# Optimization experiments

Hardware: AMD Instinct MI355X
Metric: run time of the kernel (lower is better)

The kernel has to match this reference:

```python
import jax, jax.numpy as jnp
import numpy as np

D_IN = 1024
D_OUT = 1024


def setup_inputs() -> dict:
    key = jax.random.key(0)
    k_x, k_q, k_k, k_v = jax.random.split(key, 4)
    x = jax.random.normal(k_x, (8, 2048, D_IN), dtype=jnp.float32)
    s = 1.0 / np.sqrt(D_IN)
    W_query = jax.random.uniform(k_q, (D_IN, D_OUT), jnp.float32, -s, s)
    W_key = jax.random.uniform(k_k, (D_IN, D_OUT), jnp.float32, -s, s)
    W_value = jax.random.uniform(k_v, (D_IN, D_OUT), jnp.float32, -s, s)
    return {"x": x, "W_query": W_query, "W_key": W_key, "W_value": W_value}


def reference(x, W_query, W_key, W_value):
    # x: [B, N, d_in]; weights stored as [d_in, d_out] (already transposed vs torch Linear)
    B, N, _ = x.shape
    q = x @ W_query          # [B, N, d_out]
    k = x @ W_key
    v = x @ W_value
    scores = jnp.einsum('bnd,bmd->bnm', q, k)  # [B, N, N]
    causal = jnp.tril(jnp.ones((N, N), dtype=bool))
    scores = jnp.where(causal, scores, -jnp.inf)
    weights = jax.nn.softmax(scores / np.sqrt(D_OUT), axis=-1)
    # dropout p=0.0 -> identity
    return jnp.einsum('bnm,bmd->bnd', weights, v)
```

## Files before the change

### kernel.cpp

```cpp
#include <hip/hip_runtime.h>
#include <hip/hip_bf16.h>

typedef unsigned short u16;
typedef unsigned int u32;
typedef __bf16 bf16x8 __attribute__((ext_vector_type(8)));
typedef float f32x4 __attribute__((ext_vector_type(4)));
typedef unsigned int u32x4 __attribute__((ext_vector_type(4)));

#define BATCH 8
#define SEQ   2048
#define DIM   1024
#define M_TOT (BATCH * SEQ)
#define N_QKV (3 * DIM)

#define OFF_QKV  ((size_t)0)
#define OFF_VT   ((size_t)100663296)
#define OFF_C    ((size_t)134217728)
#define OFF_XB   OFF_C
#define OFF_WT   (OFF_C + (size_t)33554432)
#define OFF_S    OFF_C

__device__ __forceinline__ u16 f32_to_bf16(float f) {
    u32 u = __builtin_bit_cast(u32, f);
    u = (u + 0x7fffu + ((u >> 16) & 1u)) >> 16;
    return (u16)u;
}

__device__ __forceinline__ float bf16_to_f32(u16 h) {
    u32 u = ((u32)h) << 16;
    return __builtin_bit_cast(float, u);
}

__device__ __forceinline__ bf16x8 lds_load8(const u16* p) {
    return __builtin_bit_cast(bf16x8, *(const u32x4*)p);
}

__device__ __forceinline__ void stage_tile64(const u16* gA, size_t lda, u16* ldsA, int tid) {
    int wv = tid >> 6;
#pragma unroll
    for (int iss = 0; iss < 4; ++iss) {
        int s = iss * 256 + tid;
        int row = s >> 3;
        int kg = (s & 7) ^ (row & 7);
        const u16* gp = gA + (size_t)row * lda + (kg << 3);
        u16* lp = ldsA + (size_t)(iss * 256 + wv * 64) * 8;
        __builtin_amdgcn_global_load_lds((const __attribute__((address_space(1))) void*)gp,
                                         (__attribute__((address_space(3))) void*)lp,
                                         16, 0, 0);
    }
}

__device__ __forceinline__ void mfma_step64(const u16* ldsA, const u16* ldsB, int tid,
                                            f32x4 acc[4][4]) {
    int lane = tid & 63;
    int wv = tid >> 6;
    int wr = (wv >> 1) * 64, wc = (wv & 1) * 64;
    int lrow = lane & 15, kgl = lane >> 4;
    int xr = lrow & 7;
#pragma unroll
    for (int ks = 0; ks < 2; ++ks) {
        int off = ((ks * 4 + kgl) ^ xr) << 3;
        bf16x8 a[4], b[4];
#pragma unroll
        for (int i = 0; i < 4; ++i) {
            a[i] = lds_load8(&ldsA[(wr + i * 16 + lrow) * 64 + off]);
            b[i] = lds_load8(&ldsB[(wc + i * 16 + lrow) * 64 + off]);
        }
#pragma unroll
        for (int i = 0; i < 4; ++i)
#pragma unroll
            for (int j = 0; j < 4; ++j)
                acc[i][j] = __builtin_amdgcn_mfma_f32_16x16x32_bf16(a[i], b[j], acc[i][j], 0, 0, 0);
    }
}

__global__ __launch_bounds__(256) void cast_x_kernel(const float* __restrict__ x,
                                                     u16* __restrict__ xb) {
    size_t g = (size_t)blockIdx.x * 256 + threadIdx.x;
    f32x4 v = ((const f32x4*)x)[g];
    u16 o[4] = {f32_to_bf16(v.x), f32_to_bf16(v.y), f32_to_bf16(v.z), f32_to_bf16(v.w)};
    *(unsigned long long*)(xb + g * 4) = *(const unsigned long long*)o;
}

__global__ __launch_bounds__(256) void transpose_w_kernel(const float* __restrict__ wq,
                                                          const float* __restrict__ wk,
                                                          const float* __restrict__ wv,
                                                          u16* __restrict__ wt) {
    __shared__ __align__(16) u16 tile[64][80];
    const float* w = blockIdx.z == 0 ? wq : (blockIdx.z == 1 ? wk : wv);
    int k0 = blockIdx.x * 64, n0 = blockIdx.y * 64;
    for (int g = threadIdx.x; g < 1024; g += 256) {
        int r = g >> 4, c = (g & 15) << 2;
        f32x4 v = *(const f32x4*)(w + (size_t)(k0 + r) * 1024 + n0 + c);
        tile[r][c + 0] = f32_to_bf16(v.x);
        tile[r][c + 1] = f32_to_bf16(v.y);
        tile[r][c + 2] = f32_to_bf16(v.z);
        tile[r][c + 3] = f32_to_bf16(v.w);
    }
    __syncthreads();
    u16* out = wt + (size_t)blockIdx.z * 1024 * 1024;
    for (int g = threadIdx.x; g < 512; g += 256) {
        int nr = g >> 3, kc = (g & 7) << 3;
        __align__(16) u16 tmp[8];
#pragma unroll
        for (int i = 0; i < 8; ++i) tmp[i] = tile[kc + i][nr];
        *(u32x4*)(out + (size_t)(n0 + nr) * 1024 + k0 + kc) = *(const u32x4*)tmp;
    }
}

__global__ __launch_bounds__(256, 2) void gemm_qkv_kernel(const u16* __restrict__ xb,
                                                          const u16* __restrict__ wt,
                                                          u16* __restrict__ qkv) {
    __shared__ __align__(16) u16 ldsA[128 * 64];
    __shared__ __align__(16) u16 ldsB[128 * 64];
    int nt = blockIdx.x, mt = blockIdx.y;
    const u16* A = xb + (size_t)mt * 128 * 1024;
    const u16* B = wt + (size_t)nt * 128 * 1024;
    int tid = threadIdx.x;
    f32x4 acc[4][4] = {};
    for (int kt = 0; kt < 16; ++kt) {
        __syncthreads();
        stage_tile64(A + kt * 64, 1024, ldsA, tid);
        stage_tile64(B + kt * 64, 1024, ldsB, tid);
        __syncthreads();
        mfma_step64(ldsA, ldsB, tid, acc);
    }
    int lane = tid & 63, wv = tid >> 6;
    int wr = (wv >> 1) * 64, wc = (wv & 1) * 64;
    int r0 = (lane >> 4) * 4, c0 = lane & 15;
    size_t mbase = (size_t)mt * 128;
    int nbase = nt * 128;
#pragma unroll
    for (int i = 0; i < 4; ++i)
#pragma unroll
        for (int j = 0; j < 4; ++j) {
            int col = nbase + wc + j * 16 + c0;
            float scale = (col < 1024) ? 0.03125f : 1.0f;
#pragma unroll
            for (int r = 0; r < 4; ++r) {
                int row = wr + i * 16 + r0 + r;
                qkv[(mbase + row) * (size_t)N_QKV + col] = f32_to_bf16(acc[i][j][r] * scale);
            }
        }
}

__global__ __launch_bounds__(256) void transpose_v_kernel(const u16* __restrict__ qkv,
                                                          u16* __restrict__ vt) {
    __shared__ __align__(16) u16 tile[64][80];
    int m0 = blockIdx.x * 64, d0 = blockIdx.y * 64, b = blockIdx.z;
    const u16* src = qkv + (size_t)b * SEQ * N_QKV + 2048;
    for (int g = threadIdx.x; g < 512; g += 256) {
        int r = g >> 3, c = (g & 7) << 3;
        *(u32x4*)&tile[r][c] = *(const u32x4*)(src + (size_t)(m0 + r) * N_QKV + d0 + c);
    }
    __syncthreads();
    u16* dst = vt + (size_t)b * DIM * SEQ;
    for (int g = threadIdx.x; g < 512; g += 256) {
        int dr = g >> 3, mc = (g & 7) << 3;
        __align__(16) u16 tmp[8];
#pragma unroll
        for (int i = 0; i < 8; ++i) tmp[i] = tile[mc + i][dr];
        *(u32x4*)(dst + (size_t)(d0 + dr) * SEQ + m0 + mc) = *(const u32x4*)tmp;
    }
}

__global__ __launch_bounds__(256, 2) void gemm_scores_kernel(const u16* __restrict__ qkv,
                                                             u16* __restrict__ S) {
    int t = blockIdx.x;
    int b = blockIdx.y;
    int ntile = (int)((sqrtf(8.0f * (float)t + 1.0f) - 1.0f) * 0.5f);
    while ((ntile + 1) * (ntile + 2) / 2 <= t) ++ntile;
    while (ntile * (ntile + 1) / 2 > t) --ntile;
    int mtile = t - ntile * (ntile + 1) / 2;
    __shared__ __align__(16) u16 ldsA[128 * 64];
    __shared__ __align__(16) u16 ldsB[128 * 64];
    const u16* A = qkv + (size_t)b * SEQ * N_QKV + (size_t)ntile * 128 * N_QKV;
    const u16* B = qkv + (size_t)b * SEQ * N_QKV + (size_t)mtile * 128 * N_QKV + 1024;
    int tid = threadIdx.x;
    f32x4 acc[4][4] = {};
    for (int kt = 0; kt < 16; ++kt) {
        __syncthreads();
        stage_tile64(A + kt * 64, N_QKV, ldsA, tid);
        stage_tile64(B + kt * 64, N_QKV, ldsB, tid);
        __syncthreads();
        mfma_step64(ldsA, ldsB, tid, acc);
    }
    u16* out = S + (size_t)b * SEQ * SEQ + (size_t)ntile * 128 * SEQ + (size_t)mtile * 128;
    int lane = tid & 63, wv = tid >> 6;
    int wr = (wv >> 1) * 64, wc = (wv & 1) * 64;
    int r0 = (lane >> 4) * 4, c0 = lane & 15;
#pragma unroll
    for (int i = 0; i < 4; ++i)
#pragma unroll
        for (int j = 0; j < 4; ++j) {
            int col = wc + j * 16 + c0;
#pragma unroll
            for (int r = 0; r < 4; ++r) {
                int row = wr + i * 16 + r0 + r;
                out[(size_t)row * SEQ + col] = f32_to_bf16(acc[i][j][r]);
            }
        }
}

__global__ __launch_bounds__(256) void softmax_kernel(u16* __restrict__ SP) {
    int gr = blockIdx.x;
    int n = gr & 2047;
    u16* s = SP + (size_t)gr * SEQ;
    __shared__ float red[4];
    int t = threadIdx.x;
    int base = t << 3;
    int len = n + 1;
    float v[8];
    float lmax = -3.0e38f;
    if (base < len) {
        u32x4 raw = *(const u32x4*)(s + base);
        const u16* h = (const u16*)&raw;
#pragma unroll
        for (int i = 0; i < 8; ++i) {
            v[i] = (base + i < len) ? bf16_to_f32(h[i]) : -3.0e38f;
            lmax = fmaxf(lmax, v[i]);
        }
    } else {
#pragma unroll
        for (int i = 0; i < 8; ++i) v[i] = -3.0e38f;
    }
#pragma unroll
    for (int off = 32; off; off >>= 1) lmax = fmaxf(lmax, __shfl_xor(lmax, off, 64));
    if ((t & 63) == 0) red[t >> 6] = lmax;
    __syncthreads();
    float gmax = fmaxf(fmaxf(red[0], red[1]), fmaxf(red[2], red[3]));
    __syncthreads();
    float lsum = 0.f;
#pragma unroll
    for (int i = 0; i < 8; ++i) {
        float e = __expf(v[i] - gmax);
        v[i] = e;
        lsum += e;
    }
#pragma unroll
    for (int off = 32; off; off >>= 1) lsum += __shfl_xor(lsum, off, 64);
    if ((t & 63) == 0) red[t >> 6] = lsum;
    __syncthreads();
    float inv = 1.0f / (red[0] + red[1] + red[2] + red[3]);
    __align__(16) u16 o[8];
#pragma unroll
    for (int i = 0; i < 8; ++i) o[i] = f32_to_bf16(v[i] * inv);
    *(u32x4*)(s + base) = *(const u32x4*)o;
}

__global__ __launch_bounds__(256, 2) void gemm_out_kernel(const u16* __restrict__ P,
                                                          const u16* __restrict__ vt,
                                                          float* __restrict__ O) {
    __shared__ __align__(16) u16 ldsA[128 * 64];
    __shared__ __align__(16) u16 ldsB[128 * 64];
    int dt = blockIdx.x, b = blockIdx.z;
    int ntile = (SEQ / 128 - 1) - blockIdx.y;
    const u16* A = P + (size_t)b * SEQ * SEQ + (size_t)ntile * 128 * SEQ;
    const u16* B = vt + (size_t)b * DIM * SEQ + (size_t)dt * 128 * SEQ;
    int tid = threadIdx.x;
    f32x4 acc[4][4] = {};
    int kTiles = ntile * 2 + 2;
    for (int kt = 0; kt < kTiles; ++kt) {
        __syncthreads();
        stage_tile64(A + kt * 64, SEQ, ldsA, tid);
        stage_tile64(B + kt * 64, SEQ, ldsB, tid);
        __syncthreads();
        mfma_step64(ldsA, ldsB, tid, acc);
    }
    float* out = O + (size_t)b * SEQ * DIM + (size_t)ntile * 128 * DIM + (size_t)dt * 128;
    int lane = tid & 63, wv = tid >> 6;
    int wr = (wv >> 1) * 64, wc = (wv & 1) * 64;
    int r0 = (lane >> 4) * 4, c0 = lane & 15;
#pragma unroll
    for (int i = 0; i < 4; ++i)
#pragma unroll
        for (int j = 0; j < 4; ++j) {
            int col = wc + j * 16 + c0;
#pragma unroll
            for (int r = 0; r < 4; ++r) {
                int row = wr + i * 16 + r0 + r;
                out[(size_t)row * DIM + col] = acc[i][j][r];
            }
        }
}

extern "C" void kernel_launch(void* const* d_in, const int* in_sizes, int n_in,
                              void* d_out, int out_size, void* d_ws, size_t ws_size,
                              hipStream_t stream) {
    const float* x = (const float*)d_in[0];
    const float* wq = (const float*)d_in[1];
    const float* wk = (const float*)d_in[2];
    const float* wv = (const float*)d_in[3];
    char* ws = (char*)d_ws;
    u16* qkv = (u16*)(ws + OFF_QKV);
    u16* vt = (u16*)(ws + OFF_VT);
    u16* xb = (u16*)(ws + OFF_XB);
    u16* wt = (u16*)(ws + OFF_WT);
    u16* S = (u16*)(ws + OFF_S);
    float* O = (float*)d_out;

    cast_x_kernel<<<M_TOT * DIM / 4 / 256, 256, 0, stream>>>(x, xb);
    transpose_w_kernel<<<dim3(16, 16, 3), 256, 0, stream>>>(wq, wk, wv, wt);
    gemm_qkv_kernel<<<dim3(N_QKV / 128, M_TOT / 128), 256, 0, stream>>>(xb, wt, qkv);
    transpose_v_kernel<<<dim3(SEQ / 64, DIM / 64, BATCH), 256, 0, stream>>>(qkv, vt);
    gemm_scores_kernel<<<dim3(136, BATCH), 256, 0, stream>>>(qkv, S);
    softmax_kernel<<<BATCH * SEQ, 256, 0, stream>>>(S);
    gemm_out_kernel<<<dim3(DIM / 128, SEQ / 128, BATCH), 256, 0, stream>>>(S, vt, O);
}
```

Measured before the change: 394.8 us.

## Use 256x256 tiles with double-buffered async LDS pipeline in all GEMMs

Replaces the 128x128 single-buffered GEMM mainloop with a 256x256, 512-thread tile and a double-buffered global_load_lds prefetch pipeline that interleaves staging with MFMA phases, using s_setprio around MFMA bursts. The QKV GEMM also gets an XCD-aware block swizzle. This aims to hide global load latency and raise arithmetic intensity per LDS byte. It uses 128KB LDS per block, which limits occupancy, and the coarser tiles mean fewer blocks (the scores GEMM drops to 36 blocks per batch), risking tail imbalance.

```diff
diff --git a/kernel.cpp b/kernel.cpp
--- a/kernel.cpp
+++ b/kernel.cpp
@@ -35,42 +35,80 @@
     return __builtin_bit_cast(bf16x8, *(const u32x4*)p);
 }
 
-__device__ __forceinline__ void stage_tile64(const u16* gA, size_t lda, u16* ldsA, int tid) {
+#define UNIT 8192
+
+__device__ __forceinline__ void stage_unit(const u16* g, size_t lda, int k0,
+                                           u16* lds, int tid) {
     int wv = tid >> 6;
 #pragma unroll
-    for (int iss = 0; iss < 4; ++iss) {
-        int s = iss * 256 + tid;
-        int row = s >> 3;
-        int kg = (s & 7) ^ (row & 7);
-        const u16* gp = gA + (size_t)row * lda + (kg << 3);
-        u16* lp = ldsA + (size_t)(iss * 256 + wv * 64) * 8;
+    for (int iss = 0; iss < 2; ++iss) {
+        int s = iss * 512 + tid;
+        int row = s >> 2;
+        int kg = (s & 3) ^ (row & 3);
+        const u16* gp = g + (size_t)row * lda + (k0 + (kg << 3));
+        u16* lp = lds + (size_t)(iss * 512 + wv * 64) * 8;
         __builtin_amdgcn_global_load_lds((const __attribute__((address_space(1))) void*)gp,
                                          (__attribute__((address_space(3))) void*)lp,
                                          16, 0, 0);
     }
 }
 
-__device__ __forceinline__ void mfma_step64(const u16* ldsA, const u16* ldsB, int tid,
-                                            f32x4 acc[4][4]) {
+template <int MH>
+__device__ __forceinline__ void mfma_phase(const u16* uA, const u16* uB, int lane,
+                                           int wm, int wn, f32x4 acc[8][4]) {
+    int lrow = lane & 15;
+    int off = (((lane >> 4) ^ (lane & 3)) << 3);
+    bf16x8 a[4], b[4];
+#pragma unroll
+    for (int i = 0; i < 4; ++i) {
+        a[i] = lds_load8(&uA[(wm * 128 + (MH * 4 + i) * 16 + lrow) * 32 + off]);
+        b[i] = lds_load8(&uB[(wn * 64 + i * 16 + lrow) * 32 + off]);
+    }
+    __builtin_amdgcn_s_setprio(1);
+#pragma unroll
+    for (int i = 0; i < 4; ++i)
+#pragma unroll
+        for (int j = 0; j < 4; ++j)
+            acc[MH * 4 + i][j] =
+                __builtin_amdgcn_mfma_f32_16x16x32_bf16(a[i], b[j], acc[MH * 4 + i][j], 0, 0, 0);
+    __builtin_amdgcn_s_setprio(0);
+}
+
+__device__ __forceinline__ void gemm_block_256(const u16* __restrict__ A, size_t lda,
+                                               const u16* __restrict__ B, size_t ldb,
+                                               int KT, u16* lds, int tid,
+                                               f32x4 acc[8][4]) {
     int lane = tid & 63;
     int wv = tid >> 6;
-    int wr = (wv >> 1) * 64, wc = (wv & 1) * 64;
-    int lrow = lane & 15, kgl = lane >> 4;
-    int xr = lrow & 7;
-#pragma unroll
-    for (int ks = 0; ks < 2; ++ks) {
-        int off = ((ks * 4 + kgl) ^ xr) << 3;
-        bf16x8 a[4], b[4];
-#pragma unroll
-        for (int i = 0; i < 4; ++i) {
-            a[i] = lds_load8(&ldsA[(wr + i * 16 + lrow) * 64 + off]);
-            b[i] = lds_load8(&ldsB[(wc + i * 16 + lrow) * 64 + off]);
-        }
-#pragma unroll
-        for (int i = 0; i < 4; ++i)
-#pragma unroll
-            for (int j = 0; j < 4; ++j)
-                acc[i][j] = __builtin_amdgcn_mfma_f32_16x16x32_bf16(a[i], b[j], acc[i][j], 0, 0, 0);
+    int wm = wv >> 2, wn = wv & 3;
+    stage_unit(A, lda, 0,  lds + 0 * UNIT, tid);
+    stage_unit(B, ldb, 0,  lds + 4 * UNIT, tid);
+    stage_unit(A, lda, 32, lds + 1 * UNIT, tid);
+    stage_unit(B, ldb, 32, lds + 5 * UNIT, tid);
+    for (int t = 0; t < KT; ++t) {
+        int p = t & 1, pn = p ^ 1;
+        int kb = (t + 1) << 6;
+        bool pf = (t + 1 < KT);
+        asm volatile("s_waitcnt vmcnt(4)" ::: "memory");
+        __builtin_amdgcn_s_barrier();
+        if (pf) stage_unit(A, lda, kb, lds + (size_t)(pn * 2) * UNIT, tid);
+        mfma_phase<0>(lds + (size_t)(p * 2) * UNIT, lds + (size_t)(4 + p * 2) * UNIT,
+                      lane, wm, wn, acc);
+        __builtin_amdgcn_s_barrier();
+        if (pf) stage_unit(B, ldb, kb, lds + (size_t)(4 + pn * 2) * UNIT, tid);
+        mfma_phase<1>(lds + (size_t)(p * 2) * UNIT, lds + (size_t)(4 + p * 2) * UNIT,
+                      lane, wm, wn, acc);
+        __builtin_amdgcn_s_barrier();
+        if (pf) { asm volatile("s_waitcnt vmcnt(4)" ::: "memory"); }
+        else    { asm volatile("s_waitcnt vmcnt(0)" ::: "memory"); }
+        __builtin_amdgcn_s_barrier();
+        if (pf) stage_unit(A, lda, kb + 32, lds + (size_t)(pn * 2 + 1) * UNIT, tid);
+        mfma_phase<0>(lds + (size_t)(p * 2 + 1) * UNIT, lds + (size_t)(4 + p * 2 + 1) * UNIT,
+                      lane, wm, wn, acc);
+        __builtin_amdgcn_s_barrier();
+        if (pf) stage_unit(B, ldb, kb + 32, lds + (size_t)(4 + pn * 2 + 1) * UNIT, tid);
+        mfma_phase<1>(lds + (size_t)(p * 2 + 1) * UNIT, lds + (size_t)(4 + p * 2 + 1) * UNIT,
+                      lane, wm, wn, acc);
     }
 }
 
@@ -108,38 +146,34 @@
     }
 }
 
-__global__ __launch_bounds__(256, 2) void gemm_qkv_kernel(const u16* __restrict__ xb,
+__global__ __launch_bounds__(512, 2) void gemm_qkv_kernel(const u16* __restrict__ xb,
                                                           const u16* __restrict__ wt,
                                                           u16* __restrict__ qkv) {
-    __shared__ __align__(16) u16 ldsA[128 * 64];
-    __shared__ __align__(16) u16 ldsB[128 * 64];
-    int nt = blockIdx.x, mt = blockIdx.y;
-    const u16* A = xb + (size_t)mt * 128 * 1024;
-    const u16* B = wt + (size_t)nt * 128 * 1024;
+    __shared__ __align__(16) u16 lds[8 * UNIT];
+    int wg = blockIdx.x;
+    int qx = gridDim.x >> 3;
+    int swz = (wg & 7) * qx + (wg >> 3);
+    int mt = swz / 12, nt = swz - mt * 12;
+    const u16* A = xb + (size_t)mt * 256 * 1024;
+    const u16* B = wt + (size_t)nt * 256 * 1024;
     int tid = threadIdx.x;
-    f32x4 acc[4][4] = {};
-    for (int kt = 0; kt < 16; ++kt) {
-        __syncthreads();
-        stage_tile64(A + kt * 64, 1024, ldsA, tid);
-        stage_tile64(B + kt * 64, 1024, ldsB, tid);
-        __syncthreads();
-        mfma_step64(ldsA, ldsB, tid, acc);
-    }
+    f32x4 acc[8][4] = {};
+    gemm_block_256(A, 1024, B, 1024, 16, lds, tid, acc);
     int lane = tid & 63, wv = tid >> 6;
-    int wr = (wv >> 1) * 64, wc = (wv & 1) * 64;
-    int r0 = (lane >> 4) * 4, c0 = lane & 15;
-    size_t mbase = (size_t)mt * 128;
-    int nbase = nt * 128;
-#pragma unroll
-    for (int i = 0; i < 4; ++i)
+    int wm = wv >> 2, wn = wv & 3;
+    int r0 = (lane >> 4) << 2, c0 = lane & 15;
+    size_t mbase = (size_t)mt * 256 + wm * 128;
+    int nbase = nt * 256 + wn * 64;
+#pragma unroll
+    for (int i = 0; i < 8; ++i)
 #pragma unroll
         for (int j = 0; j < 4; ++j) {
-            int col = nbase + wc + j * 16 + c0;
+            int col = nbase + j * 16 + c0;
             float scale = (col < 1024) ? 0.03125f : 1.0f;
 #pragma unroll
             for (int r = 0; r < 4; ++r) {
-                int row = wr + i * 16 + r0 + r;
-                qkv[(mbase + row) * (size_t)N_QKV + col] = f32_to_bf16(acc[i][j][r] * scale);
+                size_t row = mbase + i * 16 + r0 + r;
+                qkv[row * (size_t)N_QKV + col] = f32_to_bf16(acc[i][j][r] * scale);
             }
         }
 }
@@ -164,39 +198,33 @@
     }
 }
 
-__global__ __launch_bounds__(256, 2) void gemm_scores_kernel(const u16* __restrict__ qkv,
+__global__ __launch_bounds__(512, 2) void gemm_scores_kernel(const u16* __restrict__ qkv,
                                                              u16* __restrict__ S) {
+    __shared__ __align__(16) u16 lds[8 * UNIT];
     int t = blockIdx.x;
     int b = blockIdx.y;
-    int ntile = (int)((sqrtf(8.0f * (float)t + 1.0f) - 1.0f) * 0.5f);
-    while ((ntile + 1) * (ntile + 2) / 2 <= t) ++ntile;
-    while (ntile * (ntile + 1) / 2 > t) --ntile;
-    int mtile = t - ntile * (ntile + 1) / 2;
-    __shared__ __align__(16) u16 ldsA[128 * 64];
-    __shared__ __align__(16) u16 ldsB[128 * 64];
-    const u16* A = qkv + (size_t)b * SEQ * N_QKV + (size_t)ntile * 128 * N_QKV;
-    const u16* B = qkv + (size_t)b * SEQ * N_QKV + (size_t)mtile * 128 * N_QKV + 1024;
+    int ntile = 0;
+#pragma unroll
+    for (int it = 1; it < 8; ++it)
+        if ((it * (it + 1)) / 2 <= t) ntile = it;
+    int mtile = t - (ntile * (ntile + 1)) / 2;
+    const u16* A = qkv + (size_t)b * SEQ * N_QKV + (size_t)ntile * 256 * N_QKV;
+    const u16* B = qkv + (size_t)b * SEQ * N_QKV + (size_t)mtile * 256 * N_QKV + 1024;
     int tid = threadIdx.x;
-    f32x4 acc[4][4] = {};
-    for (int kt = 0; kt < 16; ++kt) {
-        __syncthreads();
-        stage_tile64(A + kt * 64, N_QKV, ldsA, tid);
-        stage_tile64(B + kt * 64, N_QKV, ldsB, tid);
-        __syncthreads();
-        mfma_step64(ldsA, ldsB, tid, acc);
-    }
-    u16* out = S + (size_t)b * SEQ * SEQ + (size_t)ntile * 128 * SEQ + (size_t)mtile * 128;
+    f32x4 acc[8][4] = {};
+    gemm_block_256(A, N_QKV, B, N_QKV, 16, lds, tid, acc);
+    u16* out = S + (size_t)b * SEQ * SEQ + (size_t)ntile * 256 * SEQ + (size_t)mtile * 256;
     int lane = tid & 63, wv = tid >> 6;
-    int wr = (wv >> 1) * 64, wc = (wv & 1) * 64;
-    int r0 = (lane >> 4) * 4, c0 = lane & 15;
-#pragma unroll
-    for (int i = 0; i < 4; ++i)
+    int wm = wv >> 2, wn = wv & 3;
+    int r0 = (lane >> 4) << 2, c0 = lane & 15;
+#pragma unroll
+    for (int i = 0; i < 8; ++i)
 #pragma unroll
         for (int j = 0; j < 4; ++j) {
-            int col = wc + j * 16 + c0;
+            int col = wn * 64 + j * 16 + c0;
 #pragma unroll
             for (int r = 0; r < 4; ++r) {
-                int row = wr + i * 16 + r0 + r;
+                int row = wm * 128 + i * 16 + r0 + r;
                 out[(size_t)row * SEQ + col] = f32_to_bf16(acc[i][j][r]);
             }
         }
@@ -248,37 +276,30 @@
     *(u32x4*)(s + base) = *(const u32x4*)o;
 }
 
-__global__ __launch_bounds__(256, 2) void gemm_out_kernel(const u16* __restrict__ P,
+__global__ __launch_bounds__(512, 2) void gemm_out_kernel(const u16* __restrict__ P,
                                                           const u16* __restrict__ vt,
                                                           float* __restrict__ O) {
-    __shared__ __align__(16) u16 ldsA[128 * 64];
-    __shared__ __align__(16) u16 ldsB[128 * 64];
+    __shared__ __align__(16) u16 lds[8 * UNIT];
     int dt = blockIdx.x, b = blockIdx.z;
-    int ntile = (SEQ / 128 - 1) - blockIdx.y;
-    const u16* A = P + (size_t)b * SEQ * SEQ + (size_t)ntile * 128 * SEQ;
-    const u16* B = vt + (size_t)b * DIM * SEQ + (size_t)dt * 128 * SEQ;
+    int ntile = (SEQ / 256 - 1) - blockIdx.y;
+    const u16* A = P + (size_t)b * SEQ * SEQ + (size_t)ntile * 256 * SEQ;
+    const u16* B = vt + (size_t)b * DIM * SEQ + (size_t)dt * 256 * SEQ;
     int tid = threadIdx.x;
-    f32x4 acc[4][4] = {};
-    int kTiles = ntile * 2 + 2;
-    for (int kt = 0; kt < kTiles; ++kt) {
-        __syncthreads();
-        stage_tile64(A + kt * 64, SEQ, ldsA, tid);
-        stage_tile64(B + kt * 64, SEQ, ldsB, tid);
-        __syncthreads();
-        mfma_step64(ldsA, ldsB, tid, acc);
-    }
-    float* out = O + (size_t)b * SEQ * DIM + (size_t)ntile * 128 * DIM + (size_t)dt * 128;
+    f32x4 acc[8][4] = {};
+    int KT = (ntile + 1) * 4;
+    gemm_block_256(A, SEQ, B, SEQ, KT, lds, tid, acc);
+    float* out = O + (size_t)b * SEQ * DIM + (size_t)ntile * 256 * DIM + (size_t)dt * 256;
     int lane = tid & 63, wv = tid >> 6;
-    int wr = (wv >> 1) * 64, wc = (wv & 1) * 64;
-    int r0 = (lane >> 4) * 4, c0 = lane & 15;
-#pragma unroll
-    for (int i = 0; i < 4; ++i)
+    int wm = wv >> 2, wn = wv & 3;
+    int r0 = (lane >> 4) << 2, c0 = lane & 15;
+#pragma unroll
+    for (int i = 0; i < 8; ++i)
 #pragma unroll
         for (int j = 0; j < 4; ++j) {
-            int col = wc + j * 16 + c0;
+            int col = wn * 64 + j * 16 + c0;
 #pragma unroll
             for (int r = 0; r < 4; ++r) {
-                int row = wr + i * 16 + r0 + r;
+                int row = wm * 128 + i * 16 + r0 + r;
                 out[(size_t)row * DIM + col] = acc[i][j][r];
             }
         }
@@ -301,9 +322,9 @@
 
     cast_x_kernel<<<M_TOT * DIM / 4 / 256, 256, 0, stream>>>(x, xb);
     transpose_w_kernel<<<dim3(16, 16, 3), 256, 0, stream>>>(wq, wk, wv, wt);
-    gemm_qkv_kernel<<<dim3(N_QKV / 128, M_TOT / 128), 256, 0, stream>>>(xb, wt, qkv);
+    gemm_qkv_kernel<<<(M_TOT / 256) * (N_QKV / 256), 512, 0, stream>>>(xb, wt, qkv);
     transpose_v_kernel<<<dim3(SEQ / 64, DIM / 64, BATCH), 256, 0, stream>>>(qkv, vt);
-    gemm_scores_kernel<<<dim3(136, BATCH), 256, 0, stream>>>(qkv, S);
+    gemm_scores_kernel<<<dim3(36, BATCH), 512, 0, stream>>>(qkv, S);
     softmax_kernel<<<BATCH * SEQ, 256, 0, stream>>>(S);
-    gemm_out_kernel<<<dim3(DIM / 128, SEQ / 128, BATCH), 256, 0, stream>>>(S, vt, O);
-}
+    gemm_out_kernel<<<dim3(DIM / 256, SEQ / 256, BATCH), 512, 0, stream>>>(S, vt, O);
+}
```

New measurement: 401.9 us. No clear change (+1.8%).

## Double-buffer LDS tiles in all GEMM kernels to overlap loads with MFMA

Applied to the files above, without the earlier changes.

Adds a shared gemm_loop_db helper that prefetches the next K-tile into a second LDS buffer while MFMAs run on the current one. Partial vmcnt waits and raw s_barrier calls replace the two __syncthreads per step in the QKV, scores and output GEMMs. The goal is to hide global-load latency behind matrix math. This doubles LDS per block to 64 KB, which can limit occupancy, and it relies on stage_tile64 issuing a fixed count of vector-memory ops. The triangular tile index in the scores kernel is also recomputed with an unrolled loop instead of sqrtf.

```diff
diff --git a/kernel.cpp b/kernel.cpp
--- a/kernel.cpp
+++ b/kernel.cpp
@@ -19,6 +19,8 @@
 #define OFF_XB   OFF_C
 #define OFF_WT   (OFF_C + (size_t)33554432)
 #define OFF_S    OFF_C
+
+#define TILE_ELEMS (128 * 64)
 
 __device__ __forceinline__ u16 f32_to_bf16(float f) {
     u32 u = __builtin_bit_cast(u32, f);
@@ -71,6 +73,31 @@
 #pragma unroll
             for (int j = 0; j < 4; ++j)
                 acc[i][j] = __builtin_amdgcn_mfma_f32_16x16x32_bf16(a[i], b[j], acc[i][j], 0, 0, 0);
+    }
+}
+
+__device__ __forceinline__ void gemm_loop_db(const u16* __restrict__ A, size_t lda,
+                                             const u16* __restrict__ B, size_t ldb,
+                                             int KT, u16* ldsA, u16* ldsB, int tid,
+                                             f32x4 acc[4][4]) {
+    stage_tile64(A, lda, ldsA, tid);
+    stage_tile64(B, ldb, ldsB, tid);
+    int cur = 0;
+    for (int t = 0; t < KT; ++t) {
+        int nxt = cur ^ 1;
+        if (t + 1 < KT) {
+            stage_tile64(A + (size_t)(t + 1) * 64, lda, ldsA + nxt * TILE_ELEMS, tid);
+            stage_tile64(B + (size_t)(t + 1) * 64, ldb, ldsB + nxt * TILE_ELEMS, tid);
+            asm volatile("s_waitcnt vmcnt(8)" ::: "memory");
+        } else {
+            asm volatile("s_waitcnt vmcnt(0)" ::: "memory");
+        }
+        __builtin_amdgcn_s_barrier();
+        __builtin_amdgcn_sched_barrier(0);
+        mfma_step64(ldsA + cur * TILE_ELEMS, ldsB + cur * TILE_ELEMS, tid, acc);
+        __builtin_amdgcn_s_barrier();
+        __builtin_amdgcn_sched_barrier(0);
+        cur = nxt;
     }
 }
 
@@ -111,20 +138,14 @@
 __global__ __launch_bounds__(256, 2) void gemm_qkv_kernel(const u16* __restrict__ xb,
                                                           const u16* __restrict__ wt,
                                                           u16* __restrict__ qkv) {
-    __shared__ __align__(16) u16 ldsA[128 * 64];
-    __shared__ __align__(16) u16 ldsB[128 * 64];
+    __shared__ __align__(16) u16 ldsA[2 * TILE_ELEMS];
+    __shared__ __align__(16) u16 ldsB[2 * TILE_ELEMS];
     int nt = blockIdx.x, mt = blockIdx.y;
     const u16* A = xb + (size_t)mt * 128 * 1024;
     const u16* B = wt + (size_t)nt * 128 * 1024;
     int tid = threadIdx.x;
     f32x4 acc[4][4] = {};
-    for (int kt = 0; kt < 16; ++kt) {
-        __syncthreads();
-        stage_tile64(A + kt * 64, 1024, ldsA, tid);
-        stage_tile64(B + kt * 64, 1024, ldsB, tid);
-        __syncthreads();
-        mfma_step64(ldsA, ldsB, tid, acc);
-    }
+    gemm_loop_db(A, 1024, B, 1024, 16, ldsA, ldsB, tid, acc);
     int lane = tid & 63, wv = tid >> 6;
     int wr = (wv >> 1) * 64, wc = (wv & 1) * 64;
     int r0 = (lane >> 4) * 4, c0 = lane & 15;
@@ -168,23 +189,18 @@
                                                              u16* __restrict__ S) {
     int t = blockIdx.x;
     int b = blockIdx.y;
-    int ntile = (int)((sqrtf(8.0f * (float)t + 1.0f) - 1.0f) * 0.5f);
-    while ((ntile + 1) * (ntile + 2) / 2 <= t) ++ntile;
-    while (ntile * (ntile + 1) / 2 > t) --ntile;
-    int mtile = t - ntile * (ntile + 1) / 2;
-    __shared__ __align__(16) u16 ldsA[128 * 64];
-    __shared__ __align__(16) u16 ldsB[128 * 64];
+    int ntile = 0;
+#pragma unroll
+    for (int it = 1; it < 16; ++it)
+        if ((it * (it + 1)) / 2 <= t) ntile = it;
+    int mtile = t - (ntile * (ntile + 1)) / 2;
+    __shared__ __align__(16) u16 ldsA[2 * TILE_ELEMS];
+    __shared__ __align__(16) u16 ldsB[2 * TILE_ELEMS];
     const u16* A = qkv + (size_t)b * SEQ * N_QKV + (size_t)ntile * 128 * N_QKV;
     const u16* B = qkv + (size_t)b * SEQ * N_QKV + (size_t)mtile * 128 * N_QKV + 1024;
     int tid = threadIdx.x;
     f32x4 acc[4][4] = {};
-    for (int kt = 0; kt < 16; ++kt) {
-        __syncthreads();
-        stage_tile64(A + kt * 64, N_QKV, ldsA, tid);
-        stage_tile64(B + kt * 64, N_QKV, ldsB, tid);
-        __syncthreads();
-        mfma_step64(ldsA, ldsB, tid, acc);
-    }
+    gemm_loop_db(A, N_QKV, B, N_QKV, 16, ldsA, ldsB, tid, acc);
     u16* out = S + (size_t)b * SEQ * SEQ + (size_t)ntile * 128 * SEQ + (size_t)mtile * 128;
     int lane = tid & 63, wv = tid >> 6;
     int wr = (wv >> 1) * 64, wc = (wv & 1) * 64;
@@ -251,8 +267,8 @@
 __global__ __launch_bounds__(256, 2) void gemm_out_kernel(const u16* __restrict__ P,
                                                           const u16* __restrict__ vt,
                                                           float* __restrict__ O) {
-    __shared__ __align__(16) u16 ldsA[128 * 64];
-    __shared__ __align__(16) u16 ldsB[128 * 64];
+    __shared__ __align__(16) u16 ldsA[2 * TILE_ELEMS];
+    __shared__ __align__(16) u16 ldsB[2 * TILE_ELEMS];
     int dt = blockIdx.x, b = blockIdx.z;
     int ntile = (SEQ / 128 - 1) - blockIdx.y;
     const u16* A = P + (size_t)b * SEQ * SEQ + (size_t)ntile * 128 * SEQ;
@@ -260,13 +276,7 @@
     int tid = threadIdx.x;
     f32x4 acc[4][4] = {};
     int kTiles = ntile * 2 + 2;
-    for (int kt = 0; kt < kTiles; ++kt) {
-        __syncthreads();
-        stage_tile64(A + kt * 64, SEQ, ldsA, tid);
-        stage_tile64(B + kt * 64, SEQ, ldsB, tid);
-        __syncthreads();
-        mfma_step64(ldsA, ldsB, tid, acc);
-    }
+    gemm_loop_db(A, SEQ, B, SEQ, kTiles, ldsA, ldsB, tid, acc);
     float* out = O + (size_t)b * SEQ * DIM + (size_t)ntile * 128 * DIM + (size_t)dt * 128;
     int lane = tid & 63, wv = tid >> 6;
     int wr = (wv >> 1) * 64, wc = (wv & 1) * 64;
```

Result: slower. 409.3 us (+3.7%).
